# Kernel tuning notes

Hardware: AMD Instinct MI355X
Metric: run time of the kernel (lower is better)

Reference implementation:

```python
import jax, jax.numpy as jnp
import numpy as np

EPS = 1e-5


def _mamba(x, in_w, conv_w, conv_b, x_w, dt_w, dt_b, A_log, D, out_w):
    # x: [B, L, d_model] -> [B, L, d_model]; mamba_ssm defaults (bias-free in/out proj)
    Bsz, L, _ = x.shape
    d_inner, d_conv = conv_w.shape
    dt_rank = dt_w.shape[1]
    N = A_log.shape[1]

    xz = x @ in_w.T                              # [B, L, 2*d_inner]
    u, z = jnp.split(xz, 2, axis=-1)

    # causal depthwise conv (torch pads both sides by d_conv-1 then slices [:L])
    uc = jnp.pad(u.transpose(0, 2, 1), ((0, 0), (0, 0), (d_conv - 1, 0)))  # [B, d, L+pad]
    uc = jax.lax.conv_general_dilated(
        uc, conv_w[:, None, :], window_strides=(1,), padding='VALID',
        feature_group_count=d_inner, dimension_numbers=('NCH', 'OIH', 'NCH'))
    u = jax.nn.silu(uc + conv_b[None, :, None]).transpose(0, 2, 1)          # [B, L, d]

    xdbc = u @ x_w.T                              # [B, L, dt_rank + 2N]
    dt, Bm, Cm = jnp.split(xdbc, [dt_rank, dt_rank + N], axis=-1)
    delta = jax.nn.softplus(dt @ dt_w.T + dt_b)   # [B, L, d]

    A = -jnp.exp(A_log)                           # [d, N]
    dA = jnp.exp(delta[..., None] * A)            # [B, L, d, N]
    dBu = delta[..., None] * Bm[:, :, None, :] * u[..., None]  # [B, L, d, N]

    def step(h, inp):
        dA_t, dBu_t, C_t = inp
        h = dA_t * h + dBu_t                      # [B, d, N]
        y = jnp.einsum('bdn,bn->bd', h, C_t)
        return h, y

    h0 = jnp.zeros((Bsz, d_inner, N), dA.dtype)
    _, ys = jax.lax.scan(step, h0,
                         (dA.transpose(1, 0, 2, 3), dBu.transpose(1, 0, 2, 3), Cm.transpose(1, 0, 2)))
    y = ys.transpose(1, 0, 2)                     # [B, L, d]
    y = (y + u * D) * jax.nn.silu(z)
    return y @ out_w.T


def reference(x, input_lengths, m, emb, conv_w, conv_b, ln_g, ln_b,
              f_in_w, f_conv_w, f_conv_b, f_x_w, f_dt_w, f_dt_b, f_A_log, f_D, f_out_w,
              b_in_w, b_conv_w, b_conv_b, b_x_w, b_dt_w, b_dt_b, b_A_log, b_D, b_out_w,
              proj_w, proj_b):
    K = conv_w.shape[-1]
    pad = (K - 1) // 2
    h = emb[x].transpose(0, 2, 1)                 # [B, C, L]
    for i in range(conv_w.shape[0]):
        h = jax.lax.conv_general_dilated(h, conv_w[i], (1,), [(pad, pad)],
                                         dimension_numbers=('NCH', 'OIH', 'NCH'))
        h = h + conv_b[i][None, :, None]
        mu = h.mean(axis=1, keepdims=True)
        var = ((h - mu) ** 2).mean(axis=1, keepdims=True)
        h = (h - mu) * jax.lax.rsqrt(var + EPS)
        h = h * ln_g[i][None, :, None] + ln_b[i][None, :, None]
        h = jnp.where(h > 0, h, 0.2 * h)          # LeakyReLU(0.2); dropout is eval no-op
        h = jnp.where(m[:, None, :], 0.0, h)
    h = h.transpose(0, 2, 1)                      # [B, L, C]
    fo = _mamba(h, f_in_w, f_conv_w, f_conv_b, f_x_w, f_dt_w, f_dt_b, f_A_log, f_D, f_out_w)
    bo = _mamba(h[:, ::-1], b_in_w, b_conv_w, b_conv_b, b_x_w, b_dt_w, b_dt_b, b_A_log, b_D, b_out_w)
    comb = jnp.concatenate([fo, bo], axis=-1) @ proj_w.T + proj_b
    return jnp.where(m[:, :, None], 0.0, comb)


def setup_inputs() -> dict:
    key = jax.random.key(0)
    ks = iter(jax.random.split(key, 40))
    B, L, C, K, depth, V = 4, 1024, 512, 5, 3, 178
    d_inner, d_state, d_conv, dt_rank = 2 * C, 16, 4, 32
    inp = {
        'x': jax.random.randint(next(ks), (B, L), 0, V),
        'input_lengths': jax.random.randint(next(ks), (B,), 1, L + 1),
        'm': jnp.zeros((B, L), dtype=bool),
        'emb': jax.random.normal(next(ks), (V, C)),
        'conv_w': jax.random.normal(next(ks), (depth, C, C, K)) * 0.05,
        'conv_b': jax.random.normal(next(ks), (depth, C)) * 0.05,
        'ln_g': jnp.ones((depth, C)),
        'ln_b': jnp.zeros((depth, C)),
        'proj_w': jax.random.normal(next(ks), (C, 2 * C)) * 0.02,
        'proj_b': jax.random.normal(next(ks), (C,)) * 0.02,
    }
    for p in ('f', 'b'):
        inp[p + '_in_w'] = jax.random.normal(next(ks), (2 * d_inner, C)) * 0.02
        inp[p + '_conv_w'] = jax.random.normal(next(ks), (d_inner, d_conv)) * 0.1
        inp[p + '_conv_b'] = jax.random.normal(next(ks), (d_inner,)) * 0.1
        inp[p + '_x_w'] = jax.random.normal(next(ks), (dt_rank + 2 * d_state, d_inner)) * 0.02
        inp[p + '_dt_w'] = jax.random.normal(next(ks), (d_inner, dt_rank)) * 0.02
        inp[p + '_dt_b'] = jax.random.normal(next(ks), (d_inner,)) * 0.1
        inp[p + '_A_log'] = jax.random.uniform(next(ks), (d_inner, d_state))
        inp[p + '_D'] = jax.random.normal(next(ks), (d_inner,)) * 0.1
        inp[p + '_out_w'] = jax.random.normal(next(ks), (C, d_inner)) * 0.02
    return inp
```

## Files before the change

### kernel.cpp

```cpp
#include <hip/hip_runtime.h>
#include <hip/hip_bf16.h>

typedef __attribute__((ext_vector_type(8))) short short8;
typedef __attribute__((ext_vector_type(4))) float f32x4;
typedef __attribute__((ext_vector_type(4))) unsigned short ushort4_t;

#define BSZ 4
#define LSEQ 1024
#define CCH 512
#define BL (BSZ*LSEQ)
#define BL2 (2*BL)
#define DI 1024
#define NST 16
#define DTR 32
#define NCH 32
#define CLEN 32

__device__ __forceinline__ float sigmoidf_(float x){ return 1.f/(1.f+__expf(-x)); }
__device__ __forceinline__ float softplus_(float x){ return x > 20.f ? x : log1pf(__expf(x)); }
__device__ __forceinline__ float fexp2_(float x){ return __builtin_amdgcn_exp2f(x); }
__device__ __forceinline__ unsigned short f2bf_(float f){
  __hip_bfloat16 h = __float2bfloat16(f); return *(unsigned short*)&h;
}

typedef const __attribute__((address_space(1))) unsigned int* gas_t;
typedef __attribute__((address_space(3))) unsigned int* las_t;
__device__ __forceinline__ void gload16(const void* g, void* l){
  __builtin_amdgcn_global_load_lds((gas_t)g, (las_t)l, 16, 0, 0);
}


struct CastEnt { const float* s; unsigned short* d; unsigned n4, acc; };
struct CastArgs { CastEnt e[9]; unsigned total4; };
__global__ void k_cast_all(CastArgs a){
  unsigned i = blockIdx.x*256 + threadIdx.x;
  if (i >= a.total4) return;
  #pragma unroll
  for (int k=0;k<9;k++){
    if (i < a.e[k].acc + a.e[k].n4){
      unsigned j = i - a.e[k].acc;
      float4 v = ((const float4*)a.e[k].s)[j];
      ushort4_t o = { f2bf_(v.x), f2bf_(v.y), f2bf_(v.z), f2bf_(v.w) };
      *(ushort4_t*)(a.e[k].d + (size_t)j*4) = o;
      return;
    }
  }
}

__global__ void k_prep_convw(const float* __restrict__ cw, __hip_bfloat16* __restrict__ wt){
  int i = blockIdx.x*256 + threadIdx.x;
  const int total = 3*CCH*CCH*5;
  if (i >= total) return;
  int j = i % (CCH*5);
  int co = (i/(CCH*5)) % CCH;
  int layer = i/(CCH*5*CCH);
  int k = j >> 9, ci = j & 511;
  wt[i] = __float2bfloat16(cw[(((size_t)layer*CCH + co)*CCH + ci)*5 + k]);
}

__global__ void k_embed(const int* __restrict__ x, const float* __restrict__ emb,
                        __hip_bfloat16* __restrict__ xpad0, __hip_bfloat16* __restrict__ xpad1){
  int i = blockIdx.x*256 + threadIdx.x;
  const int total = BSZ*(LSEQ+4)*CCH;
  const int total2 = total + BSZ*4*CCH;
  if (i >= total2) return;
  if (i >= total){
    int j = i - total;
    int c = j & (CCH-1);
    int pr = (j >> 9) & 3;
    int b = j >> 11;
    int rr = (pr < 2) ? pr : (LSEQ+2) + (pr-2);
    xpad1[((size_t)b*(LSEQ+4) + rr)*CCH + c] = __float2bfloat16(0.f);
    return;
  }
  int c = i & (CCH-1);
  int r = (i >> 9) % (LSEQ+4);
  int b = i / ((LSEQ+4)*CCH);
  float v = 0.f;
  if (r >= 2 && r < LSEQ+2){
    int tok = x[b*LSEQ + (r-2)];
    v = emb[(size_t)tok*CCH + c];
  }
  xpad0[i] = __float2bfloat16(v);
}

__global__ __launch_bounds__(256) void k_ln(
    const float* __restrict__ in, const float* __restrict__ in2,
    const float* __restrict__ g, const float* __restrict__ bb,
    const unsigned char* __restrict__ mask,
    __hip_bfloat16* __restrict__ xpad_next,
    __hip_bfloat16* __restrict__ h_enc, __hip_bfloat16* __restrict__ h_rev){
  int row = blockIdx.x;
  int b = row >> 10, l = row & 1023;
  const float* xr = in + (size_t)row*CCH;
  const float* xr2 = in2 + (size_t)row*CCH;
  int t = threadIdx.x;
  float v0 = xr[t] + xr2[t], v1 = xr[t+256] + xr2[t+256];
  float s = v0+v1, s2 = v0*v0 + v1*v1;
  #pragma unroll
  for (int off=32; off>0; off>>=1){ s += __shfl_down(s,off); s2 += __shfl_down(s2,off); }
  __shared__ float ls[8];
  if ((t&63)==0){ ls[t>>6] = s; ls[(t>>6)+4] = s2; }
  __syncthreads();
  float S  = ls[0]+ls[1]+ls[2]+ls[3];
  float S2 = ls[4]+ls[5]+ls[6]+ls[7];
  float mu = S*(1.f/CCH);
  float var = S2*(1.f/CCH) - mu*mu;
  float rs = rsqrtf(var + 1e-5f);
  bool mk = mask[row] != 0;
  #pragma unroll
  for (int e=0; e<2; e++){
    int c = t + e*256;
    float v = e ? v1 : v0;
    float h = (v-mu)*rs*g[c] + bb[c];
    h = h > 0.f ? h : 0.2f*h;
    if (mk) h = 0.f;
    __hip_bfloat16 hb = __float2bfloat16(h);
    if (xpad_next) xpad_next[((size_t)b*(LSEQ+4) + (l+2))*CCH + c] = hb;
    if (h_enc) h_enc[(size_t)row*CCH + c] = hb;
    if (h_rev) h_rev[((size_t)(b<<10) + (1023-l))*CCH + c] = hb;
  }
}

__global__ __launch_bounds__(256) void k_gemm_ksplit(
    const __hip_bfloat16* __restrict__ A, int lda,
    const __hip_bfloat16* __restrict__ W, size_t wStride,
    float* __restrict__ Cout, int ldc, int K, unsigned short* __restrict__ dtb){
  __shared__ float red[4*1024];
  int m0 = blockIdx.x << 4;
  const __hip_bfloat16* Wd = W + (size_t)(m0 >> 12)*wStride;
  int tid = threadIdx.x;
  int w = tid >> 6, lane = tid & 63;
  int r = lane & 15, kg = lane >> 4;
  int Kw = K >> 2;
  int kbase = w*Kw;

  const short* Ap = (const short*)A + (size_t)(m0 + r)*lda + kbase + kg*8;
  const short* Wp[4];
  #pragma unroll
  for (int nj=0; nj<4; nj++)
    Wp[nj] = (const short*)Wd + (size_t)(nj*16 + r)*K + kbase + kg*8;

  f32x4 acc[4];
  #pragma unroll
  for (int nj=0;nj<4;nj++) acc[nj] = (f32x4){0.f,0.f,0.f,0.f};

  for (int kk=0; kk<Kw; kk+=32){
    short8 a = *(const short8*)(Ap + kk);
    #pragma unroll
    for (int nj=0;nj<4;nj++){
      short8 wv = *(const short8*)(Wp[nj] + kk);
      acc[nj] = __builtin_amdgcn_mfma_f32_16x16x32_bf16(a, wv, acc[nj], 0,0,0);
    }
  }
  #pragma unroll
  for (int nj=0;nj<4;nj++)
    #pragma unroll
    for (int reg=0; reg<4; reg++){
      int rowt = kg*4 + reg;
      int col  = nj*16 + r;
      red[w*1024 + rowt*64 + col] = acc[nj][reg];
    }
  __syncthreads();
  int e0 = tid*4;
  f32x4 s = *(const f32x4*)&red[e0];
  #pragma unroll
  for (int ww=1; ww<4; ww++){
    f32x4 p = *(const f32x4*)&red[ww*1024 + e0];
    s.x += p.x; s.y += p.y; s.z += p.z; s.w += p.w;
  }
  int rowt = e0 >> 6, col = e0 & 63;
  *(f32x4*)&Cout[(size_t)(m0+rowt)*ldc + col] = s;
  if (col < 32){
    ushort4_t o = { f2bf_(s.x), f2bf_(s.y), f2bf_(s.z), f2bf_(s.w) };
    *(ushort4_t*)&dtb[(size_t)(m0+rowt)*32 + col] = o;
  }
}

template<bool OUTBF>
__global__ __launch_bounds__(256) void k_gemm_big(
    const __hip_bfloat16* __restrict__ A, int lda, int padExtra,
    const __hip_bfloat16* __restrict__ W, size_t wStride,
    void* __restrict__ C0, void* __restrict__ C1, int ldc, int coloff,
    int tiles_n, int baseBlocks, int totalBlocks, int Kc, int Kb,
    const float* __restrict__ bias, int biasStride, int act,
    const unsigned char* __restrict__ mask, int outRowSub, int dirColOff){
  __shared__ alignas(16) __hip_bfloat16 smem[3][6144];
  int b = blockIdx.x;
  int wg = (b & 7)*(totalBlocks >> 3) + (b >> 3);
  int seg = (wg >= baseBlocks) ? 1 : 0;
  int bid = wg - seg*baseBlocks;
  int tn = bid % tiles_n;
  int tm = bid / tiles_n;
  int m0 = tm*128, n0 = tn*64;
  int dir = m0 >> 12;
  int kOff = seg*Kc;
  const __hip_bfloat16* Wd = W + (size_t)dir*wStride;
  void* Cout = seg ? C1 : C0;
  const float* biasp = (bias && seg==0) ? bias + dir*biasStride : nullptr;

  int tid = threadIdx.x;
  int wid = tid >> 6, lane = tid & 63;
  int r = lane & 15, kg = lane >> 4;

  int sr = lane >> 2;
  int gs = (lane & 3) ^ ((sr >> 1) & 3);
  int arow0 = m0 + wid*16 + sr;
  int arow1 = arow0 + 64;
  int pa0 = arow0 + padExtra*(arow0 >> 10);
  int pa1 = arow1 + padExtra*(arow1 >> 10);
  size_t aoff0 = (size_t)pa0*lda + kOff + gs*8;
  size_t aoff1 = (size_t)pa1*lda + kOff + gs*8;
  int bcol = n0 + wid*16 + sr;
  size_t boff = (size_t)bcol*Kb + kOff + gs*8;

  int wr = wid >> 1, wc = wid & 1;
  int xs = (kg ^ ((r >> 1) & 3))*8;
  int afrag[4], bfrag[2];
  #pragma unroll
  for (int mi=0; mi<4; mi++) afrag[mi] = (wr*64 + mi*16 + r)*32 + xs;
  #pragma unroll
  for (int nj=0; nj<2; nj++) bfrag[nj] = 4096 + (wc*32 + nj*16 + r)*32 + xs;

  f32x4 acc[4][2];
  #pragma unroll
  for (int mi=0;mi<4;mi++)
    #pragma unroll
    for (int nj=0;nj<2;nj++) acc[mi][nj] = (f32x4){0.f,0.f,0.f,0.f};

  const int nt = Kc >> 5;
  auto stage = [&](int kt, int bufi){
    __hip_bfloat16* sb = &smem[bufi][0];
    int k0 = kt*32;
    gload16((const short*)A + aoff0 + k0, sb + wid*512);
    gload16((const short*)A + aoff1 + k0, sb + (wid+4)*512);
    gload16((const short*)W + (size_t)(Wd - W) + boff + k0, sb + 4096 + wid*512);
  };
  auto compute = [&](int bufi){
    const __hip_bfloat16* sb = &smem[bufi][0];
    short8 a[4], bb2[2];
    #pragma unroll
    for (int mi=0;mi<4;mi++) a[mi] = *(const short8*)&sb[afrag[mi]];
    #pragma unroll
    for (int nj=0;nj<2;nj++) bb2[nj] = *(const short8*)&sb[bfrag[nj]];
    #pragma unroll
    for (int mi=0;mi<4;mi++)
      #pragma unroll
      for (int nj=0;nj<2;nj++)
        acc[mi][nj] = __builtin_amdgcn_mfma_f32_16x16x32_bf16(a[mi], bb2[nj], acc[mi][nj], 0,0,0);
  };

  if (nt >= 3){
    stage(0, 0);
    stage(1, 1);
    int bi = 0;
    #pragma unroll 1
    for (int t=0; t<nt; t++){
      if (t+1 < nt) asm volatile("s_waitcnt vmcnt(3)" ::: "memory");
      else          asm volatile("s_waitcnt vmcnt(0)" ::: "memory");
      __builtin_amdgcn_s_barrier();
      __builtin_amdgcn_sched_barrier(0);
      if (t+2 < nt){
        int nb2 = bi + 2; if (nb2 >= 3) nb2 -= 3;
        stage(t+2, nb2);
      }
      compute(bi);
      bi = (bi+1 == 3) ? 0 : bi+1;
    }
  } else {
    for (int s=0; s<nt; s++) stage(s, s);
    asm volatile("s_waitcnt vmcnt(0)" ::: "memory");
    __builtin_amdgcn_s_barrier();
    __builtin_amdgcn_sched_barrier(0);
    for (int t=0; t<nt; t++) compute(t);
  }

  #pragma unroll
  for (int mi=0;mi<4;mi++){
    #pragma unroll
    for (int nj=0;nj<2;nj++){
      #pragma unroll
      for (int reg=0; reg<4; reg++){
        int row = m0 + wr*64 + mi*16 + kg*4 + reg;
        int col = n0 + wc*32 + nj*16 + r;
        float v = acc[mi][nj][reg];
        if (biasp) v += biasp[col];
        if (act == 1) v = softplus_(v);
        int row_out = row - dir*outRowSub;
        if (mask && mask[row_out]) v = 0.f;
        size_t o = (size_t)row_out*ldc + coloff + dir*dirColOff + col;
        if (OUTBF) ((__hip_bfloat16*)Cout)[o] = __float2bfloat16(v);
        else       ((float*)Cout)[o] = v;
      }
    }
  }
}


__global__ void k_dwconv(const float* __restrict__ xz,
                         const float* __restrict__ cw0, const float* __restrict__ cw1,
                         const float* __restrict__ cb0, const float* __restrict__ cb1,
                         float* __restrict__ u, __hip_bfloat16* __restrict__ ub){
  int i = blockIdx.x*256 + threadIdx.x;
  if (i >= BL2*DI/4) return;
  int d4 = i & (DI/4 - 1);
  int d = d4 << 2;
  int row = i >> 8;
  int dir = row >> 12;
  const float* cw = (dir ? cw1 : cw0) + d*4;
  const float* cb = (dir ? cb1 : cb0) + d;
  int l = row & 1023;
  int rb = row & ~1023;
  f32x4 cwv[4];
  #pragma unroll
  for (int j=0;j<4;j++) cwv[j] = *(const f32x4*)&cw[j*4];
  f32x4 acc = *(const f32x4*)cb;
  #pragma unroll
  for (int k=0;k<4;k++){
    int ll = l - 3 + k;
    if (ll >= 0){
      f32x4 xv = *(const f32x4*)&xz[(size_t)(rb + ll)*(2*DI) + d];
      acc.x = __fmaf_rn(cwv[0][k], xv.x, acc.x);
      acc.y = __fmaf_rn(cwv[1][k], xv.y, acc.y);
      acc.z = __fmaf_rn(cwv[2][k], xv.z, acc.z);
      acc.w = __fmaf_rn(cwv[3][k], xv.w, acc.w);
    }
  }
  f32x4 s;
  s.x = acc.x * sigmoidf_(acc.x);
  s.y = acc.y * sigmoidf_(acc.y);
  s.z = acc.z * sigmoidf_(acc.z);
  s.w = acc.w * sigmoidf_(acc.w);
  *(f32x4*)&u[(size_t)i*4] = s;
  ushort4_t o = { f2bf_(s.x), f2bf_(s.y), f2bf_(s.z), f2bf_(s.w) };
  *(ushort4_t*)((unsigned short*)ub + (size_t)i*4) = o;
}


__global__ __launch_bounds__(256) void k_scan_part(
    const float* __restrict__ Alog0, const float* __restrict__ Alog1,
    const float* __restrict__ dy, const float* __restrict__ u,
    const float* __restrict__ xdbc,
    float* __restrict__ Hp, float* __restrict__ Pp){
  __shared__ alignas(16) float Bsh[CLEN*16];
  int t = threadIdx.x;
  int dblk = blockIdx.x & 3;
  int c = (blockIdx.x >> 2) & (NCH-1);
  int b8 = blockIdx.x >> 7;
  const float* A_log = (b8 >> 2) ? Alog1 : Alog0;
  int d = dblk*256 + t;
  size_t blbase = (size_t)b8*LSEQ + (size_t)c*CLEN;
  if (t < CLEN*4){
    int l = t >> 2, q = t & 3;
    *(f32x4*)&Bsh[l*16 + q*4] = *(const f32x4*)&xdbc[(blbase+l)*64 + 32 + q*4];
  }
  float Af[16];
  #pragma unroll
  for (int n=0; n<16; n+=4){
    f32x4 a = *(const f32x4*)&A_log[(size_t)d*16 + n];
    Af[n]   = -__expf(a.x)*1.442695041f; Af[n+1] = -__expf(a.y)*1.442695041f;
    Af[n+2] = -__expf(a.z)*1.442695041f; Af[n+3] = -__expf(a.w)*1.442695041f;
  }
  float h[16];
  #pragma unroll
  for (int n=0;n<16;n++) h[n]=0.f;
  float Sdv = 0.f;
  const float* dyp = dy + blbase*DI + d;
  const float* up  = u  + blbase*DI + d;
  float dvb[2][8], uvb[2][8];
  #pragma unroll
  for (int j=0;j<8;j++){ dvb[0][j] = dyp[(size_t)j*DI]; uvb[0][j] = up[(size_t)j*DI]; }
  __syncthreads();
  #pragma unroll
  for (int g=0; g<4; g++){
    int cur = g & 1;
    if (g+1 < 4){
      int nxt = cur ^ 1;
      #pragma unroll
      for (int j=0;j<8;j++){
        size_t l = (size_t)(g+1)*8 + j;
        dvb[nxt][j] = dyp[l*DI]; uvb[nxt][j] = up[l*DI];
      }
    }
    #pragma unroll
    for (int j=0;j<8;j++){
      int l = g*8 + j;
      float dv = dvb[cur][j], uv = uvb[cur][j];
      float duv = dv*uv;
      Sdv += dv;
      #pragma unroll
      for (int n=0;n<16;n++){
        float dA = fexp2_(dv*Af[n]);
        h[n] = __fmaf_rn(dA, h[n], duv*Bsh[l*16+n]);
      }
    }
  }
  size_t pb = (((size_t)(b8*NCH + c))*DI + d)*16;
  #pragma unroll
  for (int n=0;n<16;n+=4){
    *(f32x4*)&Hp[pb+n] = (f32x4){h[n],h[n+1],h[n+2],h[n+3]};
    *(f32x4*)&Pp[pb+n] = (f32x4){fexp2_(Af[n]*Sdv), fexp2_(Af[n+1]*Sdv),
                                 fexp2_(Af[n+2]*Sdv), fexp2_(Af[n+3]*Sdv)};
  }
}

__global__ void k_scan_comb(float* __restrict__ Hp, float* __restrict__ Pp){
  int i = blockIdx.x*256 + threadIdx.x;
  if (i >= BL2*NST) return;
  int n = i & 15, row = i >> 4;
  int b8 = row >> 10, d = row & 1023;
  float hin = 0.f;
  #pragma unroll
  for (int c=0;c<NCH;c++){
    size_t idx = (((size_t)(b8*NCH + c))*DI + d)*16 + n;
    float P = Pp[idx], H = Hp[idx];
    Pp[idx] = hin;
    hin = __fmaf_rn(P, hin, H);
  }
}

__global__ __launch_bounds__(256) void k_scan_fin(
    const float* __restrict__ Alog0, const float* __restrict__ Alog1,
    const float* __restrict__ dy, const float* __restrict__ u,
    const float* __restrict__ xdbc,
    const float* __restrict__ Hin, const float* __restrict__ xz,
    const float* __restrict__ Dp0, const float* __restrict__ Dp1,
    __hip_bfloat16* __restrict__ yb){
  __shared__ alignas(16) float BCsh[CLEN*32];
  int t = threadIdx.x;
  int dblk = blockIdx.x & 3;
  int c = (blockIdx.x >> 2) & (NCH-1);
  int b8 = blockIdx.x >> 7;
  int dirb = b8 >> 2;
  const float* A_log = dirb ? Alog1 : Alog0;
  const float* Dp = dirb ? Dp1 : Dp0;
  int d = dblk*256 + t;
  size_t blbase = (size_t)b8*LSEQ + (size_t)c*CLEN;
  {
    int l = t >> 3, q = t & 7;
    *(f32x4*)&BCsh[l*32 + q*4] = *(const f32x4*)&xdbc[(blbase+l)*64 + 32 + q*4];
  }
  float Af[16];
  #pragma unroll
  for (int n=0; n<16; n+=4){
    f32x4 a = *(const f32x4*)&A_log[(size_t)d*16 + n];
    Af[n]   = -__expf(a.x)*1.442695041f; Af[n+1] = -__expf(a.y)*1.442695041f;
    Af[n+2] = -__expf(a.z)*1.442695041f; Af[n+3] = -__expf(a.w)*1.442695041f;
  }
  size_t pb = (((size_t)(b8*NCH + c))*DI + d)*16;
  float h[16];
  #pragma unroll
  for (int n=0;n<16;n+=4){
    f32x4 hv = *(const f32x4*)&Hin[pb+n];
    h[n]=hv.x; h[n+1]=hv.y; h[n+2]=hv.z; h[n+3]=hv.w;
  }
  float Dd = Dp[d];
  const float* dyp = dy + blbase*DI + d;
  const float* up  = u  + blbase*DI + d;
  const float* zp  = xz + blbase*(2*DI) + DI + d;
  float dvb[2][8], uvb[2][8], zvb[2][8];
  #pragma unroll
  for (int j=0;j<8;j++){
    dvb[0][j] = dyp[(size_t)j*DI];
    uvb[0][j] = up[(size_t)j*DI];
    zvb[0][j] = zp[(size_t)j*2*DI];
  }
  __syncthreads();
  #pragma unroll
  for (int g=0; g<4; g++){
    int cur = g & 1;
    if (g+1 < 4){
      int nxt = cur ^ 1;
      #pragma unroll
      for (int j=0;j<8;j++){
        size_t l = (size_t)(g+1)*8 + j;
        dvb[nxt][j] = dyp[l*DI];
        uvb[nxt][j] = up[l*DI];
        zvb[nxt][j] = zp[l*2*DI];
      }
    }
    #pragma unroll
    for (int j=0;j<8;j++){
      int l = g*8 + j;
      float dv = dvb[cur][j], uv = uvb[cur][j], zv = zvb[cur][j];
      float duv = dv*uv;
      float y = 0.f;
      #pragma unroll
      for (int n=0;n<16;n++){
        float dA = fexp2_(dv*Af[n]);
        h[n] = __fmaf_rn(dA, h[n], duv*BCsh[l*32+n]);
        y = __fmaf_rn(h[n], BCsh[l*32+16+n], y);
      }
      float gg = zv * sigmoidf_(zv);
      float out = __fmaf_rn(uv, Dd, y) * gg;
      yb[(blbase+l)*DI + d] = __float2bfloat16(out);
    }
  }
}


extern "C" void kernel_launch(void* const* d_in, const int* in_sizes, int n_in,
                              void* d_out, int out_size, void* d_ws, size_t ws_size,
                              hipStream_t stream){
  (void)in_sizes; (void)n_in; (void)out_size; (void)ws_size;
  const int*   x     = (const int*)d_in[0];
  const unsigned char* m = (const unsigned char*)d_in[2];
  const float* emb   = (const float*)d_in[3];
  const float* convw = (const float*)d_in[4];
  const float* convb = (const float*)d_in[5];
  const float* lng   = (const float*)d_in[6];
  const float* lnb   = (const float*)d_in[7];
  const float* projw = (const float*)d_in[8];
  const float* projb = (const float*)d_in[9];

  char* ws = (char*)d_ws;
  size_t off = 0;
  auto alloc = [&](size_t bytes)->char*{
    char* p = ws + off; off += (bytes + 255) & ~((size_t)255); return p;
  };
  auto wt_conv = (__hip_bfloat16*)alloc((size_t)3*CCH*CCH*5*2);
  auto w_in2  = (__hip_bfloat16*)alloc((size_t)2*2*DI*CCH*2);
  auto w_x2   = (__hip_bfloat16*)alloc((size_t)2*64*DI*2);
  auto w_dt2  = (__hip_bfloat16*)alloc((size_t)2*DI*DTR*2);
  auto w_out2 = (__hip_bfloat16*)alloc((size_t)2*CCH*DI*2);
  auto w_proj = (__hip_bfloat16*)alloc((size_t)CCH*1024*2);
  auto dtbias2= (float*)alloc((size_t)2*DI*4);
  auto xpad0  = (__hip_bfloat16*)alloc((size_t)BSZ*(LSEQ+4)*CCH*2);
  auto xpad1  = (__hip_bfloat16*)alloc((size_t)BSZ*(LSEQ+4)*CCH*2);
  auto scr    = (float*)alloc((size_t)8*NCH*DI*NST*4);
  auto h_cat  = (__hip_bfloat16*)alloc((size_t)BL2*CCH*2);
  auto xz2    = (float*)alloc((size_t)BL2*2*DI*4);
  auto u2     = (float*)alloc((size_t)BL2*DI*4);
  auto ub2    = (__hip_bfloat16*)alloc((size_t)BL2*DI*2);
  auto xdbc2  = (float*)alloc((size_t)BL2*64*4);
  auto dtb2   = (unsigned short*)alloc((size_t)BL2*DTR*2);
  auto dy2    = (float*)alloc((size_t)BL2*DI*4);
  auto yb2    = (__hip_bfloat16*)alloc((size_t)BL2*DI*2);
  auto fob    = (__hip_bfloat16*)alloc((size_t)BL*DI*2);
  auto Pp     = (float*)alloc((size_t)8*NCH*DI*NST*4);

  float* Hp = scr;

  auto nb = [](size_t n){ return (unsigned)((n + 255)/256); };

  k_prep_convw<<<dim3(nb((size_t)3*CCH*CCH*5)), dim3(256), 0, stream>>>(convw, wt_conv);
  {
    CastArgs ca;
    unsigned acc = 0;
    auto put = [&](int k, const void* s, void* d, unsigned n4){
      ca.e[k].s = (const float*)s; ca.e[k].d = (unsigned short*)d;
      ca.e[k].n4 = n4; ca.e[k].acc = acc; acc += n4;
    };
    for (int dir=0; dir<2; dir++){
      int base = 10 + 9*dir;
      put(dir*4+0, d_in[base+0], (unsigned short*)w_in2  + (size_t)dir*2*DI*CCH, (2*DI*CCH)/4);
      put(dir*4+1, d_in[base+3], (unsigned short*)w_x2   + (size_t)dir*64*DI,    (64*DI)/4);
      put(dir*4+2, d_in[base+4], (unsigned short*)w_dt2  + (size_t)dir*DI*DTR,   (DI*DTR)/4);
      put(dir*4+3, d_in[base+8], (unsigned short*)w_out2 + (size_t)dir*CCH*DI,   (CCH*DI)/4);
    }
    put(8, projw, w_proj, (CCH*1024)/4);
    ca.total4 = acc;
    k_cast_all<<<dim3(nb(acc)), dim3(256), 0, stream>>>(ca);
  }
  hipMemcpyAsync(dtbias2,      d_in[15], DI*sizeof(float), hipMemcpyDeviceToDevice, stream);
  hipMemcpyAsync(dtbias2 + DI, d_in[24], DI*sizeof(float), hipMemcpyDeviceToDevice, stream);

  auto gemm_big = [&](const void* A, int lda, int padE, const void* W, size_t wStride,
                  void* C0, void* C1, int ldc, int coloff,
                  int M, int N, int Kc, int Kb, int ksplit,
                  const float* bias, int biasStride, int act,
                  const unsigned char* msk, int outRowSub, int dirColOff, bool outbf){
    int tiles_n = N/64;
    int baseBlocks = (M/128)*tiles_n;
    int blocks = baseBlocks * (ksplit ? 2 : 1);
    if (outbf)
      k_gemm_big<true><<<dim3(blocks), dim3(256), 0, stream>>>((const __hip_bfloat16*)A, lda, padE,
          (const __hip_bfloat16*)W, wStride, C0, C1, ldc, coloff, tiles_n, baseBlocks, blocks,
          Kc, Kb, bias, biasStride, act, msk, outRowSub, dirColOff);
    else
      k_gemm_big<false><<<dim3(blocks), dim3(256), 0, stream>>>((const __hip_bfloat16*)A, lda, padE,
          (const __hip_bfloat16*)W, wStride, C0, C1, ldc, coloff, tiles_n, baseBlocks, blocks,
          Kc, Kb, bias, biasStride, act, msk, outRowSub, dirColOff);
  };

  k_embed<<<dim3(nb((size_t)BSZ*(LSEQ+4)*CCH + BSZ*4*CCH)), dim3(256), 0, stream>>>(x, emb, xpad0, xpad1);

  __hip_bfloat16* xp_in = xpad0;
  __hip_bfloat16* xp_out = xpad1;
  __hip_bfloat16* h_rev = h_cat + (size_t)BL*CCH;
  for (int layer=0; layer<3; layer++){
    const __hip_bfloat16* wt = wt_conv + (size_t)layer*CCH*CCH*5;
    gemm_big(xp_in, CCH, 4, wt, 0, scr, dy2, CCH, 0, BL, CCH, 1280, 2560, 1,
             convb + layer*CCH, 0, 0, nullptr, 0, 0, false);
    bool last = (layer==2);
    k_ln<<<dim3(BL), dim3(256), 0, stream>>>(scr, dy2, lng + layer*CCH, lnb + layer*CCH, m,
        last ? nullptr : xp_out, last ? h_cat : nullptr, last ? h_rev : nullptr);
    __hip_bfloat16* t2 = xp_in; xp_in = xp_out; xp_out = t2;
  }

  const float* Alog0 = (const float*)d_in[16];
  const float* Alog1 = (const float*)d_in[25];
  const float* Dp0   = (const float*)d_in[17];
  const float* Dp1   = (const float*)d_in[26];

  gemm_big(h_cat, CCH, 0, w_in2, (size_t)2*DI*CCH, xz2, xz2, 2*DI, 0,
           BL2, 2*DI, CCH, CCH, 0, nullptr, 0, 0, nullptr, 0, 0, false);
  k_dwconv<<<dim3(nb((size_t)BL2*DI/4)), dim3(256), 0, stream>>>(xz2,
      (const float*)d_in[11], (const float*)d_in[20],
      (const float*)d_in[12], (const float*)d_in[21], u2, ub2);
  k_gemm_ksplit<<<dim3(BL2/16), dim3(256), 0, stream>>>(ub2, DI, w_x2, (size_t)64*DI, xdbc2, 64, DI, dtb2);
  gemm_big(dtb2, DTR, 0, w_dt2, (size_t)DI*DTR, dy2, dy2, DI, 0,
           BL2, DI, DTR, DTR, 0, dtbias2, DI, 1, nullptr, 0, 0, false);
  k_scan_part<<<dim3(1024), dim3(256), 0, stream>>>(Alog0, Alog1, dy2, u2, xdbc2, Hp, Pp);
  k_scan_comb<<<dim3(nb((size_t)BL2*NST)), dim3(256), 0, stream>>>(Hp, Pp);
  k_scan_fin<<<dim3(1024), dim3(256), 0, stream>>>(Alog0, Alog1, dy2, u2, xdbc2, Pp, xz2, Dp0, Dp1, yb2);
  gemm_big(yb2, DI, 0, w_out2, (size_t)CCH*DI, fob, fob, DI, 0,
           BL2, CCH, DI, DI, 0, nullptr, 0, 0, nullptr, BL, 512, true);

  gemm_big(fob, DI, 0, w_proj, 0, d_out, d_out, CCH, 0,
           BL, CCH, DI, DI, 0, projb, 0, 0, m, 0, 0, false);
}
```

Measured before the change: 349.4 us.

## Double GEMM K-tile to 64 and zero-pad dt projection to K=64

The big GEMM kernel now stages a 64-wide K slice per pipeline step instead of 32. It uses a new 8-way XOR swizzle, six async loads per stage, and a doubled LDS buffer, with two MFMA passes per stage. This halves the number of barriers and waits per K, at the cost of 72KB of LDS, which may lower occupancy. Because the dt projection has K=32, its weights and activations are zero-padded to 64 through a new k_pad_dt kernel and a widened dtb write, so that GEMM still works under the new tile size.

```diff
diff --git a/kernel.cpp b/kernel.cpp
--- a/kernel.cpp
+++ b/kernel.cpp
@@ -37,7 +37,7 @@
   if (i >= a.total4) return;
   #pragma unroll
   for (int k=0;k<9;k++){
-    if (i < a.e[k].acc + a.e[k].n4){
+    if (a.e[k].n4 && i < a.e[k].acc + a.e[k].n4){
       unsigned j = i - a.e[k].acc;
       float4 v = ((const float4*)a.e[k].s)[j];
       ushort4_t o = { f2bf_(v.x), f2bf_(v.y), f2bf_(v.z), f2bf_(v.w) };
@@ -45,6 +45,15 @@
       return;
     }
   }
+}
+
+__global__ void k_pad_dt(const float* __restrict__ w0, const float* __restrict__ w1,
+                         __hip_bfloat16* __restrict__ out){
+  int i = blockIdx.x*256 + threadIdx.x;
+  if (i >= 2*DI*64) return;
+  int j = i & 63, di = (i >> 6) & (DI-1), dir = i >> 16;
+  const float* w = dir ? w1 : w0;
+  out[i] = __float2bfloat16(j < 32 ? w[di*32 + j] : 0.f);
 }
 
 __global__ void k_prep_convw(const float* __restrict__ cw, __hip_bfloat16* __restrict__ wt){
@@ -171,10 +180,10 @@
   }
   int rowt = e0 >> 6, col = e0 & 63;
   *(f32x4*)&Cout[(size_t)(m0+rowt)*ldc + col] = s;
-  if (col < 32){
-    ushort4_t o = { f2bf_(s.x), f2bf_(s.y), f2bf_(s.z), f2bf_(s.w) };
-    *(ushort4_t*)&dtb[(size_t)(m0+rowt)*32 + col] = o;
-  }
+  ushort4_t o;
+  if (col < 32) o = (ushort4_t){ f2bf_(s.x), f2bf_(s.y), f2bf_(s.z), f2bf_(s.w) };
+  else          o = (ushort4_t){ 0, 0, 0, 0 };
+  *(ushort4_t*)&dtb[(size_t)(m0+rowt)*64 + col] = o;
 }
 
 template<bool OUTBF>
@@ -185,7 +194,7 @@
     int tiles_n, int baseBlocks, int totalBlocks, int Kc, int Kb,
     const float* __restrict__ bias, int biasStride, int act,
     const unsigned char* __restrict__ mask, int outRowSub, int dirColOff){
-  __shared__ alignas(16) __hip_bfloat16 smem[3][6144];
+  __shared__ alignas(16) __hip_bfloat16 smem[3][12288];
   int b = blockIdx.x;
   int wg = (b & 7)*(totalBlocks >> 3) + (b >> 3);
   int seg = (wg >= baseBlocks) ? 1 : 0;
@@ -203,24 +212,24 @@
   int wid = tid >> 6, lane = tid & 63;
   int r = lane & 15, kg = lane >> 4;
 
-  int sr = lane >> 2;
-  int gs = (lane & 3) ^ ((sr >> 1) & 3);
-  int arow0 = m0 + wid*16 + sr;
-  int arow1 = arow0 + 64;
-  int pa0 = arow0 + padExtra*(arow0 >> 10);
-  int pa1 = arow1 + padExtra*(arow1 >> 10);
-  size_t aoff0 = (size_t)pa0*lda + kOff + gs*8;
-  size_t aoff1 = (size_t)pa1*lda + kOff + gs*8;
-  int bcol = n0 + wid*16 + sr;
-  size_t boff = (size_t)bcol*Kb + kOff + gs*8;
+  int sr = lane >> 3;
+  int gs = (lane & 7) ^ sr;
+  size_t aoffq[4]; size_t boffq[2];
+  #pragma unroll
+  for (int q=0;q<4;q++){
+    int prow = m0 + wid*8 + q*32 + sr;
+    int phys = prow + padExtra*(prow >> 10);
+    aoffq[q] = (size_t)phys*lda + kOff + gs*8;
+  }
+  #pragma unroll
+  for (int q=0;q<2;q++){
+    int bcol = n0 + wid*8 + q*32 + sr;
+    boffq[q] = (size_t)bcol*Kb + kOff + gs*8;
+  }
 
   int wr = wid >> 1, wc = wid & 1;
-  int xs = (kg ^ ((r >> 1) & 3))*8;
-  int afrag[4], bfrag[2];
-  #pragma unroll
-  for (int mi=0; mi<4; mi++) afrag[mi] = (wr*64 + mi*16 + r)*32 + xs;
-  #pragma unroll
-  for (int nj=0; nj<2; nj++) bfrag[nj] = 4096 + (wc*32 + nj*16 + r)*32 + xs;
+  int xs0 = ((kg)     ^ (r & 7))*8;
+  int xs1 = ((4 + kg) ^ (r & 7))*8;
 
   f32x4 acc[4][2];
   #pragma unroll
@@ -228,26 +237,43 @@
     #pragma unroll
     for (int nj=0;nj<2;nj++) acc[mi][nj] = (f32x4){0.f,0.f,0.f,0.f};
 
-  const int nt = Kc >> 5;
+  const int nt = Kc >> 6;
   auto stage = [&](int kt, int bufi){
     __hip_bfloat16* sb = &smem[bufi][0];
-    int k0 = kt*32;
-    gload16((const short*)A + aoff0 + k0, sb + wid*512);
-    gload16((const short*)A + aoff1 + k0, sb + (wid+4)*512);
-    gload16((const short*)W + (size_t)(Wd - W) + boff + k0, sb + 4096 + wid*512);
+    int k0 = kt*64;
+    #pragma unroll
+    for (int q=0;q<4;q++)
+      gload16((const short*)A + aoffq[q] + k0, sb + (wid*8 + q*32)*64);
+    #pragma unroll
+    for (int q=0;q<2;q++)
+      gload16((const short*)Wd + boffq[q] + k0, sb + 8192 + (wid*8 + q*32)*64);
   };
   auto compute = [&](int bufi){
     const __hip_bfloat16* sb = &smem[bufi][0];
-    short8 a[4], bb2[2];
-    #pragma unroll
-    for (int mi=0;mi<4;mi++) a[mi] = *(const short8*)&sb[afrag[mi]];
-    #pragma unroll
-    for (int nj=0;nj<2;nj++) bb2[nj] = *(const short8*)&sb[bfrag[nj]];
-    #pragma unroll
-    for (int mi=0;mi<4;mi++)
-      #pragma unroll
-      for (int nj=0;nj<2;nj++)
-        acc[mi][nj] = __builtin_amdgcn_mfma_f32_16x16x32_bf16(a[mi], bb2[nj], acc[mi][nj], 0,0,0);
+    {
+      short8 a[4], bb2[2];
+      #pragma unroll
+      for (int mi=0;mi<4;mi++) a[mi] = *(const short8*)&sb[(wr*64 + mi*16 + r)*64 + xs0];
+      #pragma unroll
+      for (int nj=0;nj<2;nj++) bb2[nj] = *(const short8*)&sb[8192 + (wc*32 + nj*16 + r)*64 + xs0];
+      #pragma unroll
+      for (int mi=0;mi<4;mi++)
+        #pragma unroll
+        for (int nj=0;nj<2;nj++)
+          acc[mi][nj] = __builtin_amdgcn_mfma_f32_16x16x32_bf16(a[mi], bb2[nj], acc[mi][nj], 0,0,0);
+    }
+    {
+      short8 a[4], bb2[2];
+      #pragma unroll
+      for (int mi=0;mi<4;mi++) a[mi] = *(const short8*)&sb[(wr*64 + mi*16 + r)*64 + xs1];
+      #pragma unroll
+      for (int nj=0;nj<2;nj++) bb2[nj] = *(const short8*)&sb[8192 + (wc*32 + nj*16 + r)*64 + xs1];
+      #pragma unroll
+      for (int mi=0;mi<4;mi++)
+        #pragma unroll
+        for (int nj=0;nj<2;nj++)
+          acc[mi][nj] = __builtin_amdgcn_mfma_f32_16x16x32_bf16(a[mi], bb2[nj], acc[mi][nj], 0,0,0);
+    }
   };
 
   if (nt >= 3){
@@ -256,7 +282,7 @@
     int bi = 0;
     #pragma unroll 1
     for (int t=0; t<nt; t++){
-      if (t+1 < nt) asm volatile("s_waitcnt vmcnt(3)" ::: "memory");
+      if (t+1 < nt) asm volatile("s_waitcnt vmcnt(6)" ::: "memory");
       else          asm volatile("s_waitcnt vmcnt(0)" ::: "memory");
       __builtin_amdgcn_s_barrier();
       __builtin_amdgcn_sched_barrier(0);
@@ -521,7 +547,7 @@
   auto wt_conv = (__hip_bfloat16*)alloc((size_t)3*CCH*CCH*5*2);
   auto w_in2  = (__hip_bfloat16*)alloc((size_t)2*2*DI*CCH*2);
   auto w_x2   = (__hip_bfloat16*)alloc((size_t)2*64*DI*2);
-  auto w_dt2  = (__hip_bfloat16*)alloc((size_t)2*DI*DTR*2);
+  auto w_dt2  = (__hip_bfloat16*)alloc((size_t)2*DI*64*2);
   auto w_out2 = (__hip_bfloat16*)alloc((size_t)2*CCH*DI*2);
   auto w_proj = (__hip_bfloat16*)alloc((size_t)CCH*1024*2);
   auto dtbias2= (float*)alloc((size_t)2*DI*4);
@@ -533,7 +559,7 @@
   auto u2     = (float*)alloc((size_t)BL2*DI*4);
   auto ub2    = (__hip_bfloat16*)alloc((size_t)BL2*DI*2);
   auto xdbc2  = (float*)alloc((size_t)BL2*64*4);
-  auto dtb2   = (unsigned short*)alloc((size_t)BL2*DTR*2);
+  auto dtb2   = (unsigned short*)alloc((size_t)BL2*64*2);
   auto dy2    = (float*)alloc((size_t)BL2*DI*4);
   auto yb2    = (__hip_bfloat16*)alloc((size_t)BL2*DI*2);
   auto fob    = (__hip_bfloat16*)alloc((size_t)BL*DI*2);
@@ -553,15 +579,18 @@
     };
     for (int dir=0; dir<2; dir++){
       int base = 10 + 9*dir;
-      put(dir*4+0, d_in[base+0], (unsigned short*)w_in2  + (size_t)dir*2*DI*CCH, (2*DI*CCH)/4);
-      put(dir*4+1, d_in[base+3], (unsigned short*)w_x2   + (size_t)dir*64*DI,    (64*DI)/4);
-      put(dir*4+2, d_in[base+4], (unsigned short*)w_dt2  + (size_t)dir*DI*DTR,   (DI*DTR)/4);
-      put(dir*4+3, d_in[base+8], (unsigned short*)w_out2 + (size_t)dir*CCH*DI,   (CCH*DI)/4);
-    }
-    put(8, projw, w_proj, (CCH*1024)/4);
+      put(dir*3+0, d_in[base+0], (unsigned short*)w_in2  + (size_t)dir*2*DI*CCH, (2*DI*CCH)/4);
+      put(dir*3+1, d_in[base+3], (unsigned short*)w_x2   + (size_t)dir*64*DI,    (64*DI)/4);
+      put(dir*3+2, d_in[base+8], (unsigned short*)w_out2 + (size_t)dir*CCH*DI,   (CCH*DI)/4);
+    }
+    put(6, projw, w_proj, (CCH*1024)/4);
+    ca.e[7].n4 = 0; ca.e[7].acc = acc; ca.e[7].s = nullptr; ca.e[7].d = nullptr;
+    ca.e[8].n4 = 0; ca.e[8].acc = acc; ca.e[8].s = nullptr; ca.e[8].d = nullptr;
     ca.total4 = acc;
     k_cast_all<<<dim3(nb(acc)), dim3(256), 0, stream>>>(ca);
   }
+  k_pad_dt<<<dim3(nb((size_t)2*DI*64)), dim3(256), 0, stream>>>(
+      (const float*)d_in[14], (const float*)d_in[23], w_dt2);
   hipMemcpyAsync(dtbias2,      d_in[15], DI*sizeof(float), hipMemcpyDeviceToDevice, stream);
   hipMemcpyAsync(dtbias2 + DI, d_in[24], DI*sizeof(float), hipMemcpyDeviceToDevice, stream);
 
@@ -609,8 +638,8 @@
       (const float*)d_in[11], (const float*)d_in[20],
       (const float*)d_in[12], (const float*)d_in[21], u2, ub2);
   k_gemm_ksplit<<<dim3(BL2/16), dim3(256), 0, stream>>>(ub2, DI, w_x2, (size_t)64*DI, xdbc2, 64, DI, dtb2);
-  gemm_big(dtb2, DTR, 0, w_dt2, (size_t)DI*DTR, dy2, dy2, DI, 0,
-           BL2, DI, DTR, DTR, 0, dtbias2, DI, 1, nullptr, 0, 0, false);
+  gemm_big(dtb2, 64, 0, w_dt2, (size_t)DI*64, dy2, dy2, DI, 0,
+           BL2, DI, 64, 64, 0, dtbias2, DI, 1, nullptr, 0, 0, false);
   k_scan_part<<<dim3(1024), dim3(256), 0, stream>>>(Alog0, Alog1, dy2, u2, xdbc2, Hp, Pp);
   k_scan_comb<<<dim3(nb((size_t)BL2*NST)), dim3(256), 0, stream>>>(Hp, Pp);
   k_scan_fin<<<dim3(1024), dim3(256), 0, stream>>>(Alog0, Alog1, dy2, u2, xdbc2, Pp, xz2, Dp0, Dp1, yb2);
```

After: 358.3 us. +2.6%, slower.
